# Kernel tuning notes

Measured on AMD Instinct MI355X. Metric: run time of the kernel, lower is better.

## Reference

```python
import jax, jax.numpy as jnp
import numpy as np

N_IMG, N_CAP, N_RGN, MAX_W, EMBED = 32, 32, 36, 50, 1024
LAMBDA_SOFTMAX = 9.0
NORM_EPS = 1e-12  # F.normalize default eps


def setup_inputs() -> dict:
    key = jax.random.key(0)
    ks = jax.random.split(key, 13)
    rgn = jax.random.normal(ks[0], (N_IMG, N_RGN, EMBED), jnp.float32)
    img = jax.random.normal(ks[1], (N_IMG, EMBED), jnp.float32)
    wrd = jax.random.normal(ks[2], (N_CAP, MAX_W, EMBED), jnp.float32)
    stc = jax.random.normal(ks[3], (N_CAP, EMBED), jnp.float32)
    # ragged caption lengths in [1, MAX_W]
    stc_lens = jax.random.randint(ks[4], (N_CAP,), 1, MAX_W + 1, dtype=jnp.int32)
    s = 1.0 / np.sqrt(EMBED)
    w_scale = jax.random.normal(ks[5], (EMBED, EMBED), jnp.float32) * s
    b_scale = jnp.zeros((EMBED,), jnp.float32)
    w_shift = jax.random.normal(ks[6], (EMBED, EMBED), jnp.float32) * s
    b_shift = jnp.zeros((EMBED,), jnp.float32)
    w1 = jax.random.normal(ks[7], (EMBED, EMBED), jnp.float32) * s
    b1 = jnp.zeros((EMBED,), jnp.float32)
    w2 = jax.random.normal(ks[8], (EMBED, EMBED), jnp.float32) * s
    b2 = jnp.zeros((EMBED,), jnp.float32)
    return dict(rgn=rgn, img=img, wrd=wrd, stc=stc, stc_lens=stc_lens,
                w_scale=w_scale, b_scale=b_scale, w_shift=w_shift, b_shift=b_shift,
                w1=w1, b1=b1, w2=w2, b2=b2)


def reference(rgn, img, wrd, stc, stc_lens, w_scale, b_scale, w_shift, b_shift, w1, b1, w2, b2):
    # rgn: (I, Q, D) regions; wrd: (C, L, D) ragged words; stc_lens: (C,)
    C, L, D = wrd.shape
    valid = jnp.arange(L)[None, :] < stc_lens[:, None]          # (C, L)
    # scores[c,i,l,q] = wrd[c,l] . rgn[i,q]  (bmm(context, queryT))
    s = jnp.einsum('cld,iqd->cilq', wrd, rgn)                   # (C, I, L, Q)
    s = jnp.where(s >= 0, s, 0.1 * s)                           # LeakyReLU(0.1)
    # L2-normalize over the query (region) axis, per (c,i,l)
    s = s / jnp.maximum(jnp.sqrt(jnp.sum(s * s, axis=3, keepdims=True)), NORM_EPS)
    # temperature softmax over valid words (ragged mask)
    logits = jnp.where(valid[:, None, :, None], s * LAMBDA_SOFTMAX, -jnp.inf)
    attn = jax.nn.softmax(logits, axis=2)                       # (C, I, L, Q)
    # weightedContext[c,i,q,d] = sum_l attn * wrd
    wei = jnp.einsum('cilq,cld->ciqd', attn, wrd)               # (C, I, Q, D)
    # FiLM-style refine
    scaling = jnp.tanh(jnp.einsum('ciqd,ed->ciqe', wei, w_scale) + b_scale)
    shifting = jnp.einsum('ciqd,ed->ciqe', wei, w_shift) + b_shift
    x = rgn[None] * scaling + shifting                          # (C, I, Q, D)
    h = jax.nn.relu(jnp.einsum('ciqd,ed->ciqe', x, w1) + b1)
    modu = jnp.einsum('ciqd,ed->ciqe', h, w2) + b2
    ref = modu + rgn[None]
    # torch cats per-caption results along dim=1 -> (I, C, Q, D)
    return jnp.transpose(ref, (1, 0, 2, 3))
```

## Files before the change

kernel.cpp:

```cpp
#include <hip/hip_runtime.h>
#include <math.h>

#define NC 32
#define NI 32
#define NL 50
#define NQ 36
#define ND 1024
#define LAMBDA 9.0f

#define BM 128
#define BN 128

typedef __attribute__((ext_vector_type(8))) short bf16x8;
typedef __attribute__((ext_vector_type(4))) float floatx4;

static __device__ __forceinline__ unsigned short f2b(float f) {
    unsigned int u = __float_as_uint(f);
    unsigned int r = (u + 0x7fffu + ((u >> 16) & 1u)) >> 16;
    return (unsigned short)r;
}
static __device__ __forceinline__ float bf2f(unsigned short u) {
    return __uint_as_float(((unsigned int)u) << 16);
}

static __device__ __forceinline__ float ftanh(float x) {
    float ax = fabsf(x);
    float e = __expf(ax + ax);
    return copysignf(1.f - 2.f / (e + 1.f), x);
}

static __device__ __forceinline__ void gload16(const unsigned short* g, unsigned short* l) {
    __builtin_amdgcn_global_load_lds(
        (const __attribute__((address_space(1))) unsigned int*)g,
        (__attribute__((address_space(3))) unsigned int*)l, 16, 0, 0);
}

struct CvtJob { const float* src; unsigned short* dst; int n2; int valid2; };
struct CvtJobs { CvtJob j[5]; };

__global__ __launch_bounds__(256) void k_cvt(CvtJobs jobs) {
    CvtJob jb = jobs.j[blockIdx.y];
    unsigned int* d32 = (unsigned int*)jb.dst;
    int stride = gridDim.x * 256;
    for (int i = blockIdx.x * 256 + threadIdx.x; i < jb.n2; i += stride) {
        unsigned int pk = 0;
        if (i < jb.valid2) {
            float2 v = ((const float2*)jb.src)[i];
            pk = (unsigned int)f2b(v.x) | ((unsigned int)f2b(v.y) << 16);
        }
        d32[i] = pk;
    }
}

struct HlJob { const float* src; unsigned short* hi; unsigned short* lo; int n2; };
struct HlJobs { HlJob j[2]; };

__global__ __launch_bounds__(256) void k_cvt_hilo(HlJobs jobs) {
    HlJob jb = jobs.j[blockIdx.y];
    unsigned int* h32 = (unsigned int*)jb.hi;
    unsigned int* l32 = (unsigned int*)jb.lo;
    int stride = gridDim.x * 256;
    for (int i = blockIdx.x * 256 + threadIdx.x; i < jb.n2; i += stride) {
        float2 v = ((const float2*)jb.src)[i];
        unsigned short h0 = f2b(v.x), h1 = f2b(v.y);
        unsigned short l0 = f2b(v.x - bf2f(h0)), l1 = f2b(v.y - bf2f(h1));
        h32[i] = (unsigned int)h0 | ((unsigned int)h1 << 16);
        l32[i] = (unsigned int)l0 | ((unsigned int)l1 << 16);
    }
}

#define SST 37
#define KVB 7168

__global__ __launch_bounds__(256) void k_attn(
    const unsigned short* __restrict__ whi, const unsigned short* __restrict__ wlo,
    const unsigned short* __restrict__ rhi, const unsigned short* __restrict__ rlo,
    const int* __restrict__ lens, unsigned short* __restrict__ attn)
{
    int bx = blockIdx.x;
    int c = bx / NI, i = bx % NI;
    __shared__ __align__(16) unsigned short KV[2][KVB];
    __shared__ float S[64 * SST];
    int t = threadIdx.x, lane = t & 63, wid = t >> 6;
    int lrow = lane & 15, quad = lane >> 4;
    int len = lens[c];

    int grow = lane >> 2;
    int ssw = ((lane & 3) ^ ((lane >> 3) & 3)) * 8;
    const unsigned short* garr = (wid == 0) ? whi : (wid == 1) ? wlo : (wid == 2) ? rhi : rlo;
    const int aoffs[4] = { 0, 2048, 4096, 5632 };
    int aoff = aoffs[wid];
    int ngroups = (wid < 2) ? 4 : 3;
    size_t gbase = (wid < 2) ? (size_t)(c * NL) * ND : (size_t)(i * NQ) * ND;

    floatx4 acc[3] = {};
    int fsw = (quad ^ ((lrow >> 1) & 3)) * 8;

    for (int j = 0; j < ngroups; ++j) {
        int row = j * 16 + grow;
        gload16(garr + gbase + (size_t)row * ND + ssw, &KV[0][aoff + j * 512 + lane * 8]);
    }
    __syncthreads();

    for (int kt = 0; kt < ND; kt += 32) {
        int cb = (kt >> 5) & 1;
        if (kt + 32 < ND) {
            for (int j = 0; j < ngroups; ++j) {
                int row = j * 16 + grow;
                gload16(garr + gbase + (size_t)row * ND + (kt + 32) + ssw,
                        &KV[cb ^ 1][aoff + j * 512 + lane * 8]);
            }
        }
        const unsigned short* KVc = KV[cb];
        bf16x8 ah = *(const bf16x8*)&KVc[(wid * 16 + lrow) * 32 + fsw];
        bf16x8 al = *(const bf16x8*)&KVc[2048 + (wid * 16 + lrow) * 32 + fsw];
#pragma unroll
        for (int nt = 0; nt < 3; ++nt) {
            bf16x8 bh = *(const bf16x8*)&KVc[4096 + (nt * 16 + lrow) * 32 + fsw];
            bf16x8 bl = *(const bf16x8*)&KVc[5632 + (nt * 16 + lrow) * 32 + fsw];
            acc[nt] = __builtin_amdgcn_mfma_f32_16x16x32_bf16(ah, bh, acc[nt], 0, 0, 0);
            acc[nt] = __builtin_amdgcn_mfma_f32_16x16x32_bf16(ah, bl, acc[nt], 0, 0, 0);
            acc[nt] = __builtin_amdgcn_mfma_f32_16x16x32_bf16(al, bh, acc[nt], 0, 0, 0);
        }
        __syncthreads();
    }
#pragma unroll
    for (int nt = 0; nt < 3; ++nt) {
        int q = nt * 16 + lrow;
        if (q < NQ) {
#pragma unroll
            for (int r = 0; r < 4; ++r) {
                int l = wid * 16 + quad * 4 + r;
                S[l * SST + q] = acc[nt][r];
            }
        }
    }
    __syncthreads();
    if (t < 200) {
        int l = t >> 2, part = t & 3;
        float lv[9];
        float ss = 0.f;
#pragma unroll
        for (int jj = 0; jj < 9; ++jj) {
            int q = part * 9 + jj;
            float v = S[l * SST + q];
            float x = (v >= 0.f) ? v : 0.1f * v;
            lv[jj] = x;
            ss += x * x;
        }
        ss += __shfl_xor(ss, 1);
        ss += __shfl_xor(ss, 2);
        float inv = LAMBDA / fmaxf(sqrtf(ss), 1e-12f);
#pragma unroll
        for (int jj = 0; jj < 9; ++jj) S[l * SST + part * 9 + jj] = lv[jj] * inv;
    }
    __syncthreads();
    if (t < 144) {
        int q = t >> 2, part = t & 3;
        int ls = part * 13;
        int le = ls + 13 < len ? ls + 13 : len;
        float m = -1e30f;
        for (int l = ls; l < le; ++l) m = fmaxf(m, S[l * SST + q]);
        m = fmaxf(m, __shfl_xor(m, 1));
        m = fmaxf(m, __shfl_xor(m, 2));
        float sum = 0.f;
        for (int l = ls; l < le; ++l) sum += __expf(S[l * SST + q] - m);
        sum += __shfl_xor(sum, 1);
        sum += __shfl_xor(sum, 2);
        float inv = 1.f / sum;
        unsigned int* o = (unsigned int*)attn + ((size_t)(c * NI + i) * NQ + q) * 32;
        int jb = part * 8;
#pragma unroll
        for (int jj = 0; jj < 8; ++jj) {
            int j = jb + jj;
            int l0 = 2 * j, l1 = 2 * j + 1;
            unsigned short a0 = (l0 < len) ? f2b(__expf(S[l0 * SST + q] - m) * inv) : (unsigned short)0;
            unsigned short a1 = (l1 < len) ? f2b(__expf(S[l1 * SST + q] - m) * inv) : (unsigned short)0;
            o[j] = (unsigned int)a0 | ((unsigned int)a1 << 16);
        }
    }
}

__global__ __launch_bounds__(256) void k_pgemm(
    const unsigned short* __restrict__ A, const unsigned short* __restrict__ B1,
    const unsigned short* __restrict__ B2, unsigned short* __restrict__ P1,
    unsigned short* __restrict__ P2)
{
    const int K = ND;
    const int BK = 32;
    int bn = blockIdx.x, bm = blockIdx.y;
    int m0 = bm * BM, n0 = bn * BN;

    __shared__ __align__(16) unsigned short smem[2][3 * 4096];

    int t = threadIdx.x, lane = t & 63, wid = t >> 6;
    int wx = wid & 1, wy = wid >> 1;
    int lrow = lane & 15, quad = lane >> 4;
    floatx4 acc1[4][4] = {}, acc2[4][4] = {};

    int srow = t >> 2, pos = t & 3;
    int ssw = (pos ^ ((srow >> 1) & 3)) * 8;
    const unsigned short* Aptr  = A  + (size_t)(m0 + srow) * K + ssw;
    const unsigned short* B1ptr = B1 + (size_t)(n0 + srow) * K + ssw;
    const unsigned short* B2ptr = B2 + (size_t)(n0 + srow) * K + ssw;
    int dst0 = srow * BK + pos * 8;
    int fsw = (quad ^ ((lrow >> 1) & 3)) * 8;

#define PG_STAGE(b, kt) { \
    unsigned short* s0 = smem[b]; \
    gload16(Aptr + (kt), &s0[dst0]); \
    gload16(Aptr + (size_t)64 * K + (kt), &s0[dst0 + 2048]); \
    gload16(B1ptr + (kt), &s0[4096 + dst0]); \
    gload16(B1ptr + (size_t)64 * K + (kt), &s0[4096 + dst0 + 2048]); \
    gload16(B2ptr + (kt), &s0[8192 + dst0]); \
    gload16(B2ptr + (size_t)64 * K + (kt), &s0[8192 + dst0 + 2048]); }

    PG_STAGE(0, 0)
    __syncthreads();

    for (int kt = 0; kt < K; kt += BK) {
        int cb = (kt >> 5) & 1;
        if (kt + BK < K) PG_STAGE(cb ^ 1, kt + BK)
        const unsigned short* At  = smem[cb];
        const unsigned short* Bt1 = smem[cb] + 4096;
        const unsigned short* Bt2 = smem[cb] + 8192;
        bf16x8 af[4], b1f[4], b2f[4];
#pragma unroll
        for (int im = 0; im < 4; ++im)
            af[im] = *(const bf16x8*)&At[(wy * 64 + im * 16 + lrow) * BK + fsw];
#pragma unroll
        for (int in = 0; in < 4; ++in) {
            b1f[in] = *(const bf16x8*)&Bt1[(wx * 64 + in * 16 + lrow) * BK + fsw];
            b2f[in] = *(const bf16x8*)&Bt2[(wx * 64 + in * 16 + lrow) * BK + fsw];
        }
#pragma unroll
        for (int im = 0; im < 4; ++im)
#pragma unroll
            for (int in = 0; in < 4; ++in) {
                acc1[im][in] = __builtin_amdgcn_mfma_f32_16x16x32_bf16(
                    af[im], b1f[in], acc1[im][in], 0, 0, 0);
                acc2[im][in] = __builtin_amdgcn_mfma_f32_16x16x32_bf16(
                    af[im], b2f[in], acc2[im][in], 0, 0, 0);
            }
        __syncthreads();
    }
#undef PG_STAGE
#pragma unroll
    for (int im = 0; im < 4; ++im)
#pragma unroll
        for (int in = 0; in < 4; ++in) {
            int n = n0 + wx * 64 + in * 16 + lrow;
#pragma unroll
            for (int r = 0; r < 4; ++r) {
                int m = m0 + wy * 64 + im * 16 + quad * 4 + r;
                int c = m / NL, l = m - c * NL;
                if (c < NC) {
                    P1[((size_t)(c * ND + n)) * 64 + l] = f2b(acc1[im][in][r]);
                    P2[((size_t)(c * ND + n)) * 64 + l] = f2b(acc2[im][in][r]);
                }
            }
        }
}

__global__ __launch_bounds__(256, 2) void k_attn_gemm(
    const unsigned short* __restrict__ attn, const unsigned short* __restrict__ Psc,
    const unsigned short* __restrict__ Psh, const float* __restrict__ bsc,
    const float* __restrict__ bsh, const float* __restrict__ rgnf,
    unsigned short* __restrict__ xbuf)
{
    int bn = blockIdx.x, bm = blockIdx.y, c = blockIdx.z;
    __shared__ __align__(16) unsigned short smem3[3 * 128 * 64];
    unsigned short* At  = smem3;
    unsigned short* B1t = smem3 + 8192;
    unsigned short* B2t = smem3 + 16384;
    unsigned short* Ct  = smem3;
    int t = threadIdx.x, lane = t & 63, wid = t >> 6;
    int wx = wid & 1, wy = wid >> 1;
    int lrow = lane & 15, quad = lane >> 4;
    int grow = lane >> 3, pos = lane & 7;

    const unsigned short* Ab  = attn + (size_t)(c * 1152 + bm * 128) * 64;
    const unsigned short* B1b = Psc + (size_t)(c * ND + bn * 128) * 64;
    const unsigned short* B2b = Psh + (size_t)(c * ND + bn * 128) * 64;
    for (int g = wid; g < 16; g += 4) {
        int row = g * 8 + grow;
        int ssw = (pos ^ (row & 7)) * 8;
        gload16(Ab + (size_t)row * 64 + ssw, &At[g * 512 + lane * 8]);
        gload16(B1b + (size_t)row * 64 + ssw, &B1t[g * 512 + lane * 8]);
        gload16(B2b + (size_t)row * 64 + ssw, &B2t[g * 512 + lane * 8]);
    }
    __syncthreads();

    floatx4 acc[4][4] = {}, acc2[4][4] = {};
#pragma unroll
    for (int kk = 0; kk < 2; ++kk) {
        int sw = ((kk * 4 + quad) ^ (lrow & 7)) * 8;
        bf16x8 af[4], b1f[4], b2f[4];
#pragma unroll
        for (int im = 0; im < 4; ++im)
            af[im] = *(const bf16x8*)&At[(wy * 64 + im * 16 + lrow) * 64 + sw];
#pragma unroll
        for (int in = 0; in < 4; ++in) {
            b1f[in] = *(const bf16x8*)&B1t[(wx * 64 + in * 16 + lrow) * 64 + sw];
            b2f[in] = *(const bf16x8*)&B2t[(wx * 64 + in * 16 + lrow) * 64 + sw];
        }
#pragma unroll
        for (int im = 0; im < 4; ++im)
#pragma unroll
            for (int in = 0; in < 4; ++in) {
                acc[im][in] = __builtin_amdgcn_mfma_f32_16x16x32_bf16(
                    af[im], b1f[in], acc[im][in], 0, 0, 0);
                acc2[im][in] = __builtin_amdgcn_mfma_f32_16x16x32_bf16(
                    af[im], b2f[in], acc2[im][in], 0, 0, 0);
            }
    }
    __syncthreads();
#pragma unroll
    for (int im = 0; im < 4; ++im)
#pragma unroll
        for (int in = 0; in < 4; ++in) {
            int n = bn * 128 + wx * 64 + in * 16 + lrow;
            float b1v = bsc[n], b2v = bsh[n];
#pragma unroll
            for (int r = 0; r < 4; ++r) {
                int row = wy * 64 + im * 16 + quad * 4 + r;
                int m = bm * 128 + row;
                int i = m / NQ, q = m - i * NQ;
                float sc = ftanh(acc[im][in][r] + b1v);
                float sh = acc2[im][in][r] + b2v;
                float rg = rgnf[(size_t)(i * NQ + q) * ND + n];
                int colc = (wx * 8 + in * 2 + (lrow >> 3)) ^ (row & 7);
                Ct[row * 128 + colc * 8 + (lrow & 7)] = f2b(rg * sc + sh);
            }
        }
    __syncthreads();
#pragma unroll
    for (int p = 0; p < 8; ++p) {
        int row = p * 16 + (t >> 4), chunk = t & 15;
        int m = bm * 128 + row;
        int i = m / NQ, q = m - i * NQ;
        size_t dr = ((size_t)(i * NC + c) * NQ + q) * ND + bn * 128 + chunk * 8;
        *(bf16x8*)&xbuf[dr] = *(const bf16x8*)&Ct[row * 128 + ((chunk ^ (row & 7)) * 8)];
    }
}

template <int MODE, int MINW>
__global__ __launch_bounds__(256, MINW) void k_gemm(
    const unsigned short* __restrict__ A, const unsigned short* __restrict__ B1,
    const float* __restrict__ bias1, const float* __restrict__ rgnf,
    void* __restrict__ outp)
{
    const int K = ND;
    extern __shared__ unsigned short smem[];
    unsigned short* Ct = smem;

    int lin = blockIdx.x;
    int xcd = lin & 7;
    int kb = lin >> 3;
    int bm = xcd * 36 + (kb >> 3);
    int bn = kb & 7;
    int m0 = bm * BM, n0 = bn * BN;

    int t = threadIdx.x;
    int lane = t & 63, wid = t >> 6;
    int wx = wid & 1, wy = wid >> 1;
    int lrow = lane & 15, quad = lane >> 4;

    floatx4 acc[4][4] = {};

    int srow = t >> 3, pos = t & 7;
    int ssw = (pos ^ (srow & 7)) * 8;
    const unsigned short* Aptr  = A  + (size_t)(m0 + srow) * K + ssw;
    const unsigned short* B1ptr = B1 + (size_t)(n0 + srow) * K + ssw;

#define G_STAGE(b, kt) { \
    unsigned short* dA = smem + (b) * 16384 + t * 8; \
    unsigned short* dB = smem + (b) * 16384 + 8192 + t * 8; \
    _Pragma("unroll") \
    for (int p = 0; p < 4; ++p) { \
        gload16(Aptr + (size_t)(p * 32) * K + (kt), dA + p * 2048); \
        gload16(B1ptr + (size_t)(p * 32) * K + (kt), dB + p * 2048); } }

    G_STAGE(0, 0)
    __syncthreads();

    for (int kt = 0; kt < K; kt += 64) {
        int cb = (kt >> 6) & 1;
        if (kt + 64 < K) G_STAGE(cb ^ 1, kt + 64)
        const unsigned short* At = smem + cb * 16384;
        const unsigned short* Bt = At + 8192;
#pragma unroll
        for (int kh = 0; kh < 2; ++kh) {
            int sw = ((kh * 4 + quad) ^ (lrow & 7)) * 8;
            bf16x8 af[4], bfr[4];
#pragma unroll
            for (int im = 0; im < 4; ++im)
                af[im] = *(const bf16x8*)&At[(wy * 64 + im * 16 + lrow) * 64 + sw];
#pragma unroll
            for (int in = 0; in < 4; ++in)
                bfr[in] = *(const bf16x8*)&Bt[(wx * 64 + in * 16 + lrow) * 64 + sw];
#pragma unroll
            for (int im = 0; im < 4; ++im)
#pragma unroll
                for (int in = 0; in < 4; ++in)
                    acc[im][in] = __builtin_amdgcn_mfma_f32_16x16x32_bf16(
                        af[im], bfr[in], acc[im][in], 0, 0, 0);
        }
        __syncthreads();
    }
#undef G_STAGE

    if constexpr (MODE == 1) {
#pragma unroll
        for (int im = 0; im < 4; ++im)
#pragma unroll
            for (int in = 0; in < 4; ++in) {
                int n = n0 + wx * 64 + in * 16 + lrow;
                float b1v = bias1[n];
#pragma unroll
                for (int r = 0; r < 4; ++r) {
                    int row = wy * 64 + im * 16 + quad * 4 + r;
                    float h = acc[im][in][r] + b1v;
                    h = h > 0.f ? h : 0.f;
                    int colc = (wx * 8 + in * 2 + (lrow >> 3)) ^ (row & 7);
                    Ct[row * 128 + colc * 8 + (lrow & 7)] = f2b(h);
                }
            }
        __syncthreads();
        unsigned short* ob = (unsigned short*)outp + (size_t)m0 * ND + n0;
#pragma unroll
        for (int p = 0; p < 8; ++p) {
            int row = p * 16 + (t >> 4), chunk = t & 15;
            *(bf16x8*)&ob[(size_t)row * ND + chunk * 8] =
                *(const bf16x8*)&Ct[row * 128 + ((chunk ^ (row & 7)) * 8)];
        }
    } else {
#pragma unroll
        for (int im = 0; im < 4; ++im)
#pragma unroll
            for (int in = 0; in < 4; ++in) {
                int n = n0 + wx * 64 + in * 16 + lrow;
                float b1v = bias1[n];
#pragma unroll
                for (int r = 0; r < 4; ++r) {
                    int m = m0 + wy * 64 + im * 16 + quad * 4 + r;
                    int i = m / (NC * NQ);
                    int q = m % NQ;
                    float rg = rgnf[(size_t)(i * NQ + q) * ND + n];
                    ((float*)outp)[(size_t)m * ND + n] = acc[im][in][r] + b1v + rg;
                }
            }
    }
}

extern "C" void kernel_launch(void* const* d_in, const int* in_sizes, int n_in,
                              void* d_out, int out_size, void* d_ws, size_t ws_size,
                              hipStream_t stream) {
    const float* rgn     = (const float*)d_in[0];
    const float* wrd     = (const float*)d_in[2];
    const int*   lens    = (const int*)d_in[4];
    const float* w_scale = (const float*)d_in[5];
    const float* b_scale = (const float*)d_in[6];
    const float* w_shift = (const float*)d_in[7];
    const float* b_shift = (const float*)d_in[8];
    const float* w1      = (const float*)d_in[9];
    const float* b1      = (const float*)d_in[10];
    const float* w2      = (const float*)d_in[11];
    const float* b2      = (const float*)d_in[12];
    float* outf = (float*)d_out;

    char* ws = (char*)d_ws;
    unsigned short* wsc_bf = (unsigned short*)(ws + 0);
    unsigned short* wsh_bf = (unsigned short*)(ws + 2097152);
    unsigned short* w1_bf  = (unsigned short*)(ws + 4194304);
    unsigned short* w2_bf  = (unsigned short*)(ws + 6291456);
    unsigned short* wrd_bf = (unsigned short*)(ws + 8388608);
    unsigned short* attn   = (unsigned short*)(ws + 11796480);
    unsigned short* P_sct  = (unsigned short*)(ws + 16515072);
    unsigned short* P_sht  = (unsigned short*)(ws + 20709376);
    unsigned short* wrd_hi = (unsigned short*)(ws + 24903680);
    unsigned short* wrd_lo = (unsigned short*)(ws + 28209152);
    unsigned short* rgn_hi = (unsigned short*)(ws + 31514624);
    unsigned short* rgn_lo = (unsigned short*)(ws + 33898496);
    unsigned short* hbuf   = (unsigned short*)(ws + 8388608);
    unsigned short* xbuf   = (unsigned short*)d_out;

    static int s_attr = []() {
        hipFuncSetAttribute((const void*)k_gemm<1, 2>,
                            hipFuncAttributeMaxDynamicSharedMemorySize, 65536);
        hipFuncSetAttribute((const void*)k_gemm<2, 2>,
                            hipFuncAttributeMaxDynamicSharedMemorySize, 65536);
        return 0;
    }();
    (void)s_attr;

    CvtJobs jobs;
    jobs.j[0] = { w_scale, wsc_bf, ND * ND / 2, ND * ND / 2 };
    jobs.j[1] = { w_shift, wsh_bf, ND * ND / 2, ND * ND / 2 };
    jobs.j[2] = { w1,      w1_bf,  ND * ND / 2, ND * ND / 2 };
    jobs.j[3] = { w2,      w2_bf,  ND * ND / 2, ND * ND / 2 };
    jobs.j[4] = { wrd,     wrd_bf, 1664 * ND / 2, NC * NL * ND / 2 };
    k_cvt<<<dim3(128, 5), 256, 0, stream>>>(jobs);

    HlJobs hjobs;
    hjobs.j[0] = { wrd, wrd_hi, wrd_lo, NC * NL * ND / 2 };
    hjobs.j[1] = { rgn, rgn_hi, rgn_lo, NI * NQ * ND / 2 };
    k_cvt_hilo<<<dim3(128, 2), 256, 0, stream>>>(hjobs);

    k_attn<<<NC * NI, 256, 0, stream>>>(wrd_hi, wrd_lo, rgn_hi, rgn_lo, lens, attn);

    k_pgemm<<<dim3(8, 13), 256, 0, stream>>>(wrd_bf, wsc_bf, wsh_bf, P_sct, P_sht);

    k_attn_gemm<<<dim3(8, 9, 32), 256, 0, stream>>>(attn, P_sct, P_sht,
                                                    b_scale, b_shift, rgn, xbuf);

    k_gemm<1, 2><<<2304, 256, 65536, stream>>>(xbuf, w1_bf, b1, rgn, hbuf);
    k_gemm<2, 2><<<2304, 256, 65536, stream>>>(hbuf, w2_bf, b2, rgn, outf);
}
```

Baseline: 495.7 us.

## Single-buffer GEMM LDS to raise occupancy and reuse wrd_hi for pgemm

The main GEMM kernels drop double-buffered dynamic LDS (64 KB) for a single static 32 KB buffer, loading each k-tile and syncing before compute. The aim is more resident blocks per CU, to hide latency through occupancy instead of software prefetch. Separately, the bf16 conversion of wrd is removed and pgemm reads the existing wrd_hi buffer instead, cutting one conversion job. This loses load/compute overlap within a block. It also assumes wrd_hi is laid out and padded like wrd_bf was (1664 rows), which may not hold.

```diff
diff --git a/kernel.cpp b/kernel.cpp
--- a/kernel.cpp
+++ b/kernel.cpp
@@ -36,7 +36,7 @@
 }
 
 struct CvtJob { const float* src; unsigned short* dst; int n2; int valid2; };
-struct CvtJobs { CvtJob j[5]; };
+struct CvtJobs { CvtJob j[4]; };
 
 __global__ __launch_bounds__(256) void k_cvt(CvtJobs jobs) {
     CvtJob jb = jobs.j[blockIdx.y];
@@ -351,9 +351,6 @@
     void* __restrict__ outp)
 {
     const int K = ND;
-    extern __shared__ unsigned short smem[];
-    unsigned short* Ct = smem;
-
     int lin = blockIdx.x;
     int xcd = lin & 7;
     int kb = lin >> 3;
@@ -361,6 +358,11 @@
     int bn = kb & 7;
     int m0 = bm * BM, n0 = bn * BN;
 
+    __shared__ __align__(16) unsigned short smem[2 * 128 * 64];
+    unsigned short* At = smem;
+    unsigned short* Bt = smem + 8192;
+    unsigned short* Ct = smem;
+
     int t = threadIdx.x;
     int lane = t & 63, wid = t >> 6;
     int wx = wid & 1, wy = wid >> 1;
@@ -372,23 +374,16 @@
     int ssw = (pos ^ (srow & 7)) * 8;
     const unsigned short* Aptr  = A  + (size_t)(m0 + srow) * K + ssw;
     const unsigned short* B1ptr = B1 + (size_t)(n0 + srow) * K + ssw;
-
-#define G_STAGE(b, kt) { \
-    unsigned short* dA = smem + (b) * 16384 + t * 8; \
-    unsigned short* dB = smem + (b) * 16384 + 8192 + t * 8; \
-    _Pragma("unroll") \
-    for (int p = 0; p < 4; ++p) { \
-        gload16(Aptr + (size_t)(p * 32) * K + (kt), dA + p * 2048); \
-        gload16(B1ptr + (size_t)(p * 32) * K + (kt), dB + p * 2048); } }
-
-    G_STAGE(0, 0)
-    __syncthreads();
+    unsigned short* ldA = At + t * 8;
+    unsigned short* ldB = Bt + t * 8;
 
     for (int kt = 0; kt < K; kt += 64) {
-        int cb = (kt >> 6) & 1;
-        if (kt + 64 < K) G_STAGE(cb ^ 1, kt + 64)
-        const unsigned short* At = smem + cb * 16384;
-        const unsigned short* Bt = At + 8192;
+#pragma unroll
+        for (int p = 0; p < 4; ++p) {
+            gload16(Aptr + (size_t)(p * 32) * K + kt, ldA + p * 2048);
+            gload16(B1ptr + (size_t)(p * 32) * K + kt, ldB + p * 2048);
+        }
+        __syncthreads();
 #pragma unroll
         for (int kh = 0; kh < 2; ++kh) {
             int sw = ((kh * 4 + quad) ^ (lrow & 7)) * 8;
@@ -408,7 +403,6 @@
         }
         __syncthreads();
     }
-#undef G_STAGE
 
     if constexpr (MODE == 1) {
 #pragma unroll
@@ -474,7 +468,6 @@
     unsigned short* wsh_bf = (unsigned short*)(ws + 2097152);
     unsigned short* w1_bf  = (unsigned short*)(ws + 4194304);
     unsigned short* w2_bf  = (unsigned short*)(ws + 6291456);
-    unsigned short* wrd_bf = (unsigned short*)(ws + 8388608);
     unsigned short* attn   = (unsigned short*)(ws + 11796480);
     unsigned short* P_sct  = (unsigned short*)(ws + 16515072);
     unsigned short* P_sht  = (unsigned short*)(ws + 20709376);
@@ -485,22 +478,12 @@
     unsigned short* hbuf   = (unsigned short*)(ws + 8388608);
     unsigned short* xbuf   = (unsigned short*)d_out;
 
-    static int s_attr = []() {
-        hipFuncSetAttribute((const void*)k_gemm<1, 2>,
-                            hipFuncAttributeMaxDynamicSharedMemorySize, 65536);
-        hipFuncSetAttribute((const void*)k_gemm<2, 2>,
-                            hipFuncAttributeMaxDynamicSharedMemorySize, 65536);
-        return 0;
-    }();
-    (void)s_attr;
-
     CvtJobs jobs;
     jobs.j[0] = { w_scale, wsc_bf, ND * ND / 2, ND * ND / 2 };
     jobs.j[1] = { w_shift, wsh_bf, ND * ND / 2, ND * ND / 2 };
     jobs.j[2] = { w1,      w1_bf,  ND * ND / 2, ND * ND / 2 };
     jobs.j[3] = { w2,      w2_bf,  ND * ND / 2, ND * ND / 2 };
-    jobs.j[4] = { wrd,     wrd_bf, 1664 * ND / 2, NC * NL * ND / 2 };
-    k_cvt<<<dim3(128, 5), 256, 0, stream>>>(jobs);
+    k_cvt<<<dim3(128, 4), 256, 0, stream>>>(jobs);
 
     HlJobs hjobs;
     hjobs.j[0] = { wrd, wrd_hi, wrd_lo, NC * NL * ND / 2 };
@@ -509,11 +492,11 @@
 
     k_attn<<<NC * NI, 256, 0, stream>>>(wrd_hi, wrd_lo, rgn_hi, rgn_lo, lens, attn);
 
-    k_pgemm<<<dim3(8, 13), 256, 0, stream>>>(wrd_bf, wsc_bf, wsh_bf, P_sct, P_sht);
+    k_pgemm<<<dim3(8, 13), 256, 0, stream>>>(wrd_hi, wsc_bf, wsh_bf, P_sct, P_sht);
 
     k_attn_gemm<<<dim3(8, 9, 32), 256, 0, stream>>>(attn, P_sct, P_sht,
                                                     b_scale, b_shift, rgn, xbuf);
 
-    k_gemm<1, 2><<<2304, 256, 65536, stream>>>(xbuf, w1_bf, b1, rgn, hbuf);
-    k_gemm<2, 2><<<2304, 256, 65536, stream>>>(hbuf, w2_bf, b2, rgn, outf);
-}
+    k_gemm<1, 2><<<2304, 256, 0, stream>>>(xbuf, w1_bf, b1, rgn, hbuf);
+    k_gemm<2, 2><<<2304, 256, 0, stream>>>(hbuf, w2_bf, b2, rgn, outf);
+}
```

Result: faster. 472.2 us (-4.7%).
